# Kernel optimization log

Hardware: AMD Instinct MI355X
Metric: run time of the kernel (lower is better)

## Reference

```python
import jax, jax.numpy as jnp
import numpy as np

N = 50000      # nodes
E = 800000     # edges per relation (avg degree 16)
D = 128        # in_feat == out_feat
H = 4          # num_heads
DH = D // H    # head dim = 32
NEG_SLOPE = 0.2  # DGL GATConv default


def setup_inputs() -> dict:
    key = jax.random.key(0)
    ks = jax.random.split(key, 12)
    inp = {
        "x": jax.random.normal(ks[0], (N, D), jnp.float32),
        "W_r0": jax.random.normal(ks[1], (D, D), jnp.float32) * (1.0 / np.sqrt(D)),
        "attn_l_r0": jax.random.normal(ks[2], (H, DH), jnp.float32),
        "attn_r_r0": jax.random.normal(ks[3], (H, DH), jnp.float32),
        "W_r1": jax.random.normal(ks[4], (D, D), jnp.float32) * (1.0 / np.sqrt(D)),
        "attn_l_r1": jax.random.normal(ks[5], (H, DH), jnp.float32),
        "attn_r_r1": jax.random.normal(ks[6], (H, DH), jnp.float32),
        "loop_weight": jax.random.normal(ks[7], (D, D), jnp.float32) * (1.0 / np.sqrt(D)),
        "h_bias": jnp.zeros((D,), jnp.float32),
        "src_r0": jax.random.randint(ks[8], (E,), 0, N, jnp.int32),
        "dst_r0": jax.random.randint(ks[9], (E,), 0, N, jnp.int32),
        "src_r1": jax.random.randint(ks[10], (E,), 0, N, jnp.int32),
        "dst_r1": jax.random.randint(ks[11], (E,), 0, N, jnp.int32),
    }
    return inp


def _gat_conv(x, W, attn_l, attn_r, src, dst):
    """One DGL-style GATConv (no bias, no conv activation). Returns [N,H,DH]."""
    feat = (x @ W).reshape(N, H, DH)                 # projected features
    el = jnp.einsum('nhd,hd->nh', feat, attn_l)      # [N,H] attn on source
    er = jnp.einsum('nhd,hd->nh', feat, attn_r)      # [N,H] attn on dest
    e = jax.nn.leaky_relu(el[src] + er[dst], NEG_SLOPE)  # [E,H]
    # edge softmax over incoming edges of each dst node (stable)
    emax = jax.ops.segment_max(e, dst, num_segments=N)   # [N,H]
    ex = jnp.exp(e - emax[dst])                          # [E,H]
    denom = jax.ops.segment_sum(ex, dst, num_segments=N) # [N,H]
    alpha = ex / denom[dst]                              # [E,H]
    msg = feat[src] * alpha[:, :, None]                  # [E,H,DH]
    return jax.ops.segment_sum(msg, dst, num_segments=N) # [N,H,DH]


def reference(x, W_r0, attn_l_r0, attn_r_r0, W_r1, attn_l_r1, attn_r_r1,
              loop_weight, h_bias, src_r0, dst_r0, src_r1, dst_r1):
    # HeteroGraphConv with default 'sum' cross-relation aggregation
    h = _gat_conv(x, W_r0, attn_l_r0, attn_r_r0, src_r0, dst_r0) \
      + _gat_conv(x, W_r1, attn_l_r1, attn_r_r1, src_r1, dst_r1)
    h = h.reshape(N, H * DH)          # flatten heads -> [N, out_feat]
    h = h + x @ loop_weight           # self loop
    h = h + h_bias                    # bias
    h = jax.nn.relu(h)                # activation (dropout=0, no norm, no FFN)
    return h
```

## Files before the change

kernel.cpp:

```cpp
#include <hip/hip_runtime.h>
#include <hip/hip_bf16.h>

#define NN 50000
#define EE 800000
#define DD 128
#define HH 4
#define NEG_SLOPE 0.2f

#define BSH 9
#define NBUCK 98
#define CH 8192
#define NBLK 98
#define NSEG (2 * NBUCK * NBLK)
#define BKB (2 * NBLK)
#define PJB ((NN + 127) / 128)

typedef __attribute__((ext_vector_type(8))) short bf16x8;
typedef __attribute__((ext_vector_type(4))) float f32x4;
typedef __attribute__((ext_vector_type(8))) unsigned short ushrt8;

static __device__ __forceinline__ float bf2f(ushort u) {
    union { unsigned int ui; float f; } v; v.ui = ((unsigned int)u) << 16; return v.f;
}
static __device__ __forceinline__ void split1(float v, ushort& h, ushort& l) {
    __hip_bfloat16 hb = __float2bfloat16(v);
    float hf = __bfloat162float(hb);
    __hip_bfloat16 lb = __float2bfloat16(v - hf);
    h = *(ushort*)&hb; l = *(ushort*)&lb;
}

#define XB 6250
#define WB 192
__global__ __launch_bounds__(256) void prep_kernel(
    const float* __restrict__ x,
    const float* __restrict__ W0, const float* __restrict__ W1,
    const float* __restrict__ Wl,
    const int* __restrict__ dst0, const int* __restrict__ dst1,
    ushort* __restrict__ xh, ushort* __restrict__ xl, ushort* __restrict__ wt,
    int* __restrict__ hist)
{
    const int b = blockIdx.x;
    const int t = threadIdx.x;
    if (b < XB) {
        int i = b * 256 + t;
        float4 v = ((const float4*)x)[i];
        ushort4 h, l;
        split1(v.x, h.x, l.x); split1(v.y, h.y, l.y);
        split1(v.z, h.z, l.z); split1(v.w, h.w, l.w);
        *(ushort4*)&xh[(size_t)i * 4] = h;
        *(ushort4*)&xl[(size_t)i * 4] = l;
    } else if (b < XB + WB) {
        int idx = (b - XB) * 256 + t;
        int m = idx >> 14, e = idx & 16383;
        const float* W = (m == 0) ? W0 : (m == 1) ? W1 : Wl;
        int k = e >> 7, n = e & 127;
        ushort h, l; split1(W[e], h, l);
        int q = m * 4 + (k >> 5);
        int kin8 = (k >> 3) & 3, ke = k & 7;
        int sw = n & 7;
        size_t base = (size_t)q * 8192 + n * 64;
        wt[base + (((0 | kin8) ^ sw) << 3) + ke] = h;
        wt[base + (((4 | kin8) ^ sw) << 3) + ke] = l;
    } else {
        __shared__ int cnt[NBUCK];
        int hb = b - XB - WB;
        int rel = hb >= NBLK;
        int ci = hb - rel * NBLK;
        const int* __restrict__ dstA = rel ? dst1 : dst0;
        if (t < NBUCK) cnt[t] = 0;
        __syncthreads();
        int lo = ci * CH, hi = min(lo + CH, EE);
        for (int i = lo + t; i < hi; i += 256)
            atomicAdd(&cnt[dstA[i] >> BSH], 1);
        __syncthreads();
        if (t < NBUCK)
            hist[((rel * NBUCK) + t) * NBLK + ci] = cnt[t];
    }
}

__global__ __launch_bounds__(256) void scan_kernel(
    const int* __restrict__ hist, int* __restrict__ base)
{
    __shared__ int wq[4];
    const int t = threadIdx.x;
    const int lane = t & 63, wv = t >> 6;
    const int st = t * 76;
    const int en = min(st + 76, NSEG);
    int sum = 0;
    for (int i = st; i < en; ++i) sum += hist[i];
    int incl = sum;
    #pragma unroll
    for (int off = 1; off < 64; off <<= 1) {
        int u = __shfl_up(incl, off);
        if (lane >= off) incl += u;
    }
    if (lane == 63) wq[wv] = incl;
    __syncthreads();
    int woff = 0;
    #pragma unroll
    for (int w = 0; w < 4; ++w) woff += (w < wv) ? wq[w] : 0;
    int run = woff + incl - sum;
    for (int i = st; i < en; ++i) { base[i] = run; run += hist[i]; }
}

__global__ __launch_bounds__(256) void projbucket_kernel(
    const int* __restrict__ src0, const int* __restrict__ dst0,
    const int* __restrict__ src1, const int* __restrict__ dst1,
    const int* __restrict__ base, unsigned int* __restrict__ pk,
    const ushort* __restrict__ xh, const ushort* __restrict__ xl,
    const ushort* __restrict__ wt,
    const float* __restrict__ al0, const float* __restrict__ ar0,
    const float* __restrict__ al1, const float* __restrict__ ar1,
    const float* __restrict__ bias,
    ushort* __restrict__ fb0, ushort* __restrict__ fb1,
    float* __restrict__ el0, float* __restrict__ er0,
    float* __restrict__ el1, float* __restrict__ er1,
    float* __restrict__ out)
{
    __shared__ ushort lds[2][8192];
    const int t = threadIdx.x;

    if (blockIdx.x < BKB) {
        int* cnt = (int*)&lds[0][0];
        int* bs  = cnt + 128;
        const int hb = blockIdx.x;
        const int rel = hb >= NBLK;
        const int ci = hb - rel * NBLK;
        const int* __restrict__ srcA = rel ? src1 : src0;
        const int* __restrict__ dstA = rel ? dst1 : dst0;
        if (t < NBUCK) {
            cnt[t] = 0;
            bs[t] = base[((rel * NBUCK) + t) * NBLK + ci];
        }
        __syncthreads();
        int lo = ci * CH, hi = min(lo + CH, EE);
        for (int i = lo + t; i < hi; i += 256) {
            int dd = dstA[i], ss = srcA[i];
            int bk = dd >> BSH;
            int rk = atomicAdd(&cnt[bk], 1);
            pk[bs[bk] + rk] = (unsigned int)ss | ((unsigned int)(dd & 511) << 17);
        }
        return;
    }

    const int pb = blockIdx.x - BKB;
    const int lane = t & 63, wave = t >> 6;
    const int l15 = lane & 15, lg = lane >> 4;
    const int rb = pb * 128 + wave * 32;

    int ra0 = rb + l15;      if (ra0 > NN - 1) ra0 = NN - 1;
    int ra1 = rb + 16 + l15; if (ra1 > NN - 1) ra1 = NN - 1;
    const int kb = lg * 8;

    bf16x8 Ah0[4], Av0[4], Ah1[4], Av1[4];
    #pragma unroll
    for (int kc = 0; kc < 4; ++kc) {
        Ah0[kc] = *(const bf16x8*)&xh[(size_t)ra0 * DD + kc * 32 + kb];
        Av0[kc] = *(const bf16x8*)&xl[(size_t)ra0 * DD + kc * 32 + kb];
        Ah1[kc] = *(const bf16x8*)&xh[(size_t)ra1 * DD + kc * 32 + kb];
        Av1[kc] = *(const bf16x8*)&xl[(size_t)ra1 * DD + kc * 32 + kb];
    }

    {
        const bf16x8* g = (const bf16x8*)wt;
        bf16x8* L = (bf16x8*)lds[0];
        #pragma unroll
        for (int i = 0; i < 4; ++i) L[t + i * 256] = g[t + i * 256];
    }

    for (int m = 0; m < 3; ++m) {
        f32x4 acc0[8], acc1[8];
        #pragma unroll
        for (int nt = 0; nt < 8; ++nt) {
            acc0[nt] = (f32x4){0.f, 0.f, 0.f, 0.f};
            acc1[nt] = (f32x4){0.f, 0.f, 0.f, 0.f};
        }

        #pragma unroll
        for (int kc = 0; kc < 4; ++kc) {
            const int q = m * 4 + kc;
            __syncthreads();
            bf16x8 st0, st1, st2, st3;
            const bool hasNext = (q < 11);
            if (hasNext) {
                const bf16x8* g = (const bf16x8*)(wt + (size_t)(q + 1) * 8192);
                st0 = g[t]; st1 = g[t + 256]; st2 = g[t + 512]; st3 = g[t + 768];
            }
            const ushort* __restrict__ L = lds[kc & 1];
            #pragma unroll
            for (int nt = 0; nt < 8; ++nt) {
                const int n = nt * 16 + l15;
                const int sw = n & 7;
                bf16x8 bh = *(const bf16x8*)&L[n * 64 + (((0 | lg) ^ sw) << 3)];
                bf16x8 bv = *(const bf16x8*)&L[n * 64 + (((4 | lg) ^ sw) << 3)];
                acc0[nt] = __builtin_amdgcn_mfma_f32_16x16x32_bf16(Ah0[kc], bh, acc0[nt], 0, 0, 0);
                acc0[nt] = __builtin_amdgcn_mfma_f32_16x16x32_bf16(Ah0[kc], bv, acc0[nt], 0, 0, 0);
                acc0[nt] = __builtin_amdgcn_mfma_f32_16x16x32_bf16(Av0[kc], bh, acc0[nt], 0, 0, 0);
                acc1[nt] = __builtin_amdgcn_mfma_f32_16x16x32_bf16(Ah1[kc], bh, acc1[nt], 0, 0, 0);
                acc1[nt] = __builtin_amdgcn_mfma_f32_16x16x32_bf16(Ah1[kc], bv, acc1[nt], 0, 0, 0);
                acc1[nt] = __builtin_amdgcn_mfma_f32_16x16x32_bf16(Av1[kc], bh, acc1[nt], 0, 0, 0);
            }
            if (hasNext) {
                bf16x8* Lw = (bf16x8*)lds[(kc & 1) ^ 1];
                Lw[t] = st0; Lw[t + 256] = st1; Lw[t + 512] = st2; Lw[t + 768] = st3;
            }
        }

        if (m < 2) {
            ushort* __restrict__ fb = m ? fb1 : fb0;
            const float* __restrict__ alm = m ? al1 : al0;
            const float* __restrict__ arm = m ? ar1 : ar0;
            float* __restrict__ elm = m ? el1 : el0;
            float* __restrict__ erm = m ? er1 : er0;
            #pragma unroll
            for (int tt = 0; tt < 2; ++tt) {
                float pl[4][4], pr[4][4];
                #pragma unroll
                for (int r = 0; r < 4; ++r)
                    #pragma unroll
                    for (int h = 0; h < 4; ++h) { pl[r][h] = 0.f; pr[r][h] = 0.f; }
                #pragma unroll
                for (int nt = 0; nt < 8; ++nt) {
                    const int col = nt * 16 + l15;
                    const float wlv = alm[col], wrv = arm[col];
                    #pragma unroll
                    for (int r = 0; r < 4; ++r) {
                        const float v = tt ? acc1[nt][r] : acc0[nt][r];
                        pl[r][nt >> 1] += v * wlv;
                        pr[r][nt >> 1] += v * wrv;
                        const int row = rb + tt * 16 + lg * 4 + r;
                        if (row < NN) {
                            __hip_bfloat16 hb = __float2bfloat16(v);
                            fb[(size_t)row * DD + col] = *(ushort*)&hb;
                        }
                    }
                }
                #pragma unroll
                for (int msk = 1; msk < 16; msk <<= 1)
                    #pragma unroll
                    for (int r = 0; r < 4; ++r)
                        #pragma unroll
                        for (int h = 0; h < 4; ++h) {
                            pl[r][h] += __shfl_xor(pl[r][h], msk);
                            pr[r][h] += __shfl_xor(pr[r][h], msk);
                        }
                if (l15 < 4) {
                    #pragma unroll
                    for (int r = 0; r < 4; ++r) {
                        const int row = rb + tt * 16 + lg * 4 + r;
                        if (row < NN) {
                            const float plv = l15 == 0 ? pl[r][0] : l15 == 1 ? pl[r][1]
                                            : l15 == 2 ? pl[r][2] : pl[r][3];
                            const float prv = l15 == 0 ? pr[r][0] : l15 == 1 ? pr[r][1]
                                            : l15 == 2 ? pr[r][2] : pr[r][3];
                            elm[(size_t)row * 4 + l15] = plv;
                            erm[(size_t)row * 4 + l15] = prv;
                        }
                    }
                }
            }
        } else {
            #pragma unroll
            for (int tt = 0; tt < 2; ++tt)
                #pragma unroll
                for (int nt = 0; nt < 8; ++nt) {
                    const int col = nt * 16 + l15;
                    const float bv = bias[col];
                    #pragma unroll
                    for (int r = 0; r < 4; ++r) {
                        const int row = rb + tt * 16 + lg * 4 + r;
                        const float v = tt ? acc1[nt][r] : acc0[nt][r];
                        if (row < NN) out[(size_t)row * DD + col] = v + bv;
                    }
                }
        }
    }
}

__global__ __launch_bounds__(256) void sort_kernel(
    const unsigned int* __restrict__ pk, const int* __restrict__ base,
    int* __restrict__ row0, int* __restrict__ row1, int* __restrict__ list)
{
    __shared__ int cnt[512];
    __shared__ int offs[512];
    __shared__ int wq[4];
    const int hb = blockIdx.x;
    const int t = threadIdx.x;
    const int lane = t & 63, wv = t >> 6;
    const int rel = hb >= NBUCK;
    const int bk = hb - rel * NBUCK;

    const int fs = base[((rel * NBUCK) + bk) * NBLK];
    const int fe = (rel == 1 && bk == NBUCK - 1) ? 2 * EE
                 : base[((rel * NBUCK) + bk + 1) * NBLK];

    cnt[t] = 0; cnt[t + 256] = 0;
    __syncthreads();
    for (int i = fs + t; i < fe; i += 256)
        atomicAdd(&cnt[pk[i] >> 17], 1);
    __syncthreads();

    int a = cnt[2 * t], bvl = cnt[2 * t + 1];
    int ps = a + bvl;
    int incl = ps;
    #pragma unroll
    for (int off = 1; off < 64; off <<= 1) {
        int u = __shfl_up(incl, off);
        if (lane >= off) incl += u;
    }
    if (lane == 63) wq[wv] = incl;
    __syncthreads();
    int woff = 0;
    #pragma unroll
    for (int w = 0; w < 4; ++w) woff += (w < wv) ? wq[w] : 0;
    int excl = woff + incl - ps;
    offs[2 * t] = excl;
    offs[2 * t + 1] = excl + a;
    __syncthreads();

    int* __restrict__ row = rel ? row1 : row0;
    const int fsLocal = fs - (rel ? EE : 0);
    const int d0 = bk << BSH;
    for (int j = t; j < 512; j += 256) {
        int d = d0 + j;
        if (d < NN) row[d] = fsLocal + offs[j] + cnt[j];
    }
    __syncthreads();

    for (int i = fs + t; i < fe; i += 256) {
        unsigned int u = pk[i];
        int ld = u >> 17;
        int p = atomicAdd(&offs[ld], 1);
        list[fs + p] = (int)(u & 0x1FFFF);
    }
}

__global__ __launch_bounds__(256) void agg_kernel(
    const int* __restrict__ row0, const int* __restrict__ list0,
    const float* __restrict__ el0, const float* __restrict__ er0,
    const int* __restrict__ row1, const int* __restrict__ list1,
    const float* __restrict__ el1, const float* __restrict__ er1,
    const ushort* __restrict__ fb0, const ushort* __restrict__ fb1,
    float* __restrict__ out)
{
    const int d = blockIdx.x * 4 + (threadIdx.x >> 6);
    const int lane = threadIdx.x & 63;
    if (d >= NN) return;
    const int g = lane >> 4;
    const int l16 = lane & 15;
    const int c = l16 * 8;
    const int h = l16 >> 2;

    float tot[8] = {0.f, 0.f, 0.f, 0.f, 0.f, 0.f, 0.f, 0.f};

    #pragma unroll
    for (int rel = 0; rel < 2; ++rel) {
        const int* __restrict__ rowA = rel ? row1 : row0;
        const int* __restrict__ lst  = rel ? list1 : list0;
        const float* __restrict__ elA = rel ? el1 : el0;
        const float* __restrict__ erA = rel ? er1 : er0;
        const ushort* __restrict__ fbA = rel ? fb1 : fb0;

        const int s0 = d ? rowA[d - 1] : 0, e0 = rowA[d];
        const float erh = erA[(size_t)d * 4 + h];
        float acc[8] = {0.f, 0.f, 0.f, 0.f, 0.f, 0.f, 0.f, 0.f};
        float den = 0.f;

        int i = s0 + g;
        float elvA = 0.f;
        ushrt8 fA = (ushrt8){0, 0, 0, 0, 0, 0, 0, 0};
        if (i < e0) {
            int s = lst[i];
            elvA = elA[(size_t)s * 4 + h];
            fA = *(const ushrt8*)&fbA[(size_t)s * DD + c];
        }
        while (i < e0) {
            const int inext = i + 4;
            float elvB = 0.f;
            ushrt8 fB = (ushrt8){0, 0, 0, 0, 0, 0, 0, 0};
            if (inext < e0) {
                int s = lst[inext];
                elvB = elA[(size_t)s * 4 + h];
                fB = *(const ushrt8*)&fbA[(size_t)s * DD + c];
            }
            float ev = elvA + erh;
            ev = ev > 0.f ? ev : NEG_SLOPE * ev;
            float w = __expf(ev);
            den += w;
            #pragma unroll
            for (int q = 0; q < 8; ++q) acc[q] += w * bf2f(fA[q]);
            i = inext; elvA = elvB; fA = fB;
        }

        den += __shfl_xor(den, 16); den += __shfl_xor(den, 32);
        #pragma unroll
        for (int q = 0; q < 8; ++q) {
            acc[q] += __shfl_xor(acc[q], 16);
            acc[q] += __shfl_xor(acc[q], 32);
        }
        if (e0 > s0) {
            float inv = 1.f / den;
            #pragma unroll
            for (int q = 0; q < 8; ++q) tot[q] += acc[q] * inv;
        }
    }

    if (g == 0) {
        float4 o1 = *(float4*)&out[(size_t)d * DD + c];
        float4 o2 = *(float4*)&out[(size_t)d * DD + c + 4];
        o1.x = fmaxf(o1.x + tot[0], 0.f); o1.y = fmaxf(o1.y + tot[1], 0.f);
        o1.z = fmaxf(o1.z + tot[2], 0.f); o1.w = fmaxf(o1.w + tot[3], 0.f);
        o2.x = fmaxf(o2.x + tot[4], 0.f); o2.y = fmaxf(o2.y + tot[5], 0.f);
        o2.z = fmaxf(o2.z + tot[6], 0.f); o2.w = fmaxf(o2.w + tot[7], 0.f);
        *(float4*)&out[(size_t)d * DD + c] = o1;
        *(float4*)&out[(size_t)d * DD + c + 4] = o2;
    }
}

extern "C" void kernel_launch(void* const* d_in, const int* in_sizes, int n_in,
                              void* d_out, int out_size, void* d_ws, size_t ws_size,
                              hipStream_t stream)
{
    const float* x    = (const float*)d_in[0];
    const float* W0   = (const float*)d_in[1];
    const float* al0  = (const float*)d_in[2];
    const float* ar0  = (const float*)d_in[3];
    const float* W1   = (const float*)d_in[4];
    const float* al1  = (const float*)d_in[5];
    const float* ar1  = (const float*)d_in[6];
    const float* Wl   = (const float*)d_in[7];
    const float* bias = (const float*)d_in[8];
    const int* src0   = (const int*)d_in[9];
    const int* dst0   = (const int*)d_in[10];
    const int* src1   = (const int*)d_in[11];
    const int* dst1   = (const int*)d_in[12];
    float* out = (float*)d_out;

    ushort* wsu = (ushort*)d_ws;
    ushort* xh  = wsu;
    ushort* xl  = xh + (size_t)NN * DD;
    ushort* fb0 = xl + (size_t)NN * DD;
    ushort* fb1 = fb0 + (size_t)NN * DD;
    ushort* wt  = fb1 + (size_t)NN * DD;
    float* fbase = (float*)(wt + 12 * 8192);
    float* el0  = fbase;
    float* er0  = el0 + (size_t)NN * HH;
    float* el1  = er0 + (size_t)NN * HH;
    float* er1  = el1 + (size_t)NN * HH;
    int* hist   = (int*)(er1 + (size_t)NN * HH);
    int* base   = hist + NSEG;
    int* row0   = base + NSEG;
    int* row1   = row0 + NN;
    unsigned int* pk = (unsigned int*)(row1 + NN);
    int* list   = (int*)(pk + (size_t)2 * EE);
    int* list0  = list;
    int* list1  = list + EE;

    prep_kernel<<<dim3(XB + WB + 2 * NBLK), dim3(256), 0, stream>>>(
        x, W0, W1, Wl, dst0, dst1, xh, xl, wt, hist);

    scan_kernel<<<dim3(1), dim3(256), 0, stream>>>(hist, base);

    projbucket_kernel<<<dim3(BKB + PJB), dim3(256), 0, stream>>>(
        src0, dst0, src1, dst1, base, pk,
        xh, xl, wt, al0, ar0, al1, ar1, bias,
        fb0, fb1, el0, er0, el1, er1, out);

    sort_kernel<<<dim3(2 * NBUCK), dim3(256), 0, stream>>>(
        pk, base, row0, row1, list);

    agg_kernel<<<dim3((NN + 3) / 4), dim3(256), 0, stream>>>(
        row0, list0, el0, er0, row1, list1, el1, er1, fb0, fb1, out);
}
```

Baseline: 217.2 us.

## Precompute attention logits via W·a vectors and fuse softmax into sort

Folds attn_l/attn_r into the projection weights, so el/er come from x times precomputed 128-vectors in a separate light kernel rather than the MFMA epilogue. The edge softmax (exp, per-destination denominator, alpha) moves into the sort blocks, which now run concurrently with the projection GEMM in one launch. The aggregation reads precomputed alpha per edge instead of recomputing exp and denominators, and the x bf16 split moves inline into the GEMM so the separate x conversion pass and its buffers go away. This costs extra global traffic for the edge weight and alpha buffers (16 bytes per edge each), plus shared-memory float atomics, and el/er are computed with a different summation order.

After: 236.4 us. 8.9% more time.

```diff
diff --git a/kernel.cpp b/kernel.cpp
--- a/kernel.cpp
+++ b/kernel.cpp
@@ -13,7 +13,10 @@
 #define NBLK 98
 #define NSEG (2 * NBUCK * NBLK)
 #define BKB (2 * NBLK)
+#define SORTB (2 * NBUCK)
+#define ELRB 3125
 #define PJB ((NN + 127) / 128)
+#define WB 192
 
 typedef __attribute__((ext_vector_type(8))) short bf16x8;
 typedef __attribute__((ext_vector_type(4))) float f32x4;
@@ -29,28 +32,18 @@
     h = *(ushort*)&hb; l = *(ushort*)&lb;
 }
 
-#define XB 6250
-#define WB 192
 __global__ __launch_bounds__(256) void prep_kernel(
-    const float* __restrict__ x,
     const float* __restrict__ W0, const float* __restrict__ W1,
     const float* __restrict__ Wl,
+    const float* __restrict__ al0, const float* __restrict__ ar0,
+    const float* __restrict__ al1, const float* __restrict__ ar1,
     const int* __restrict__ dst0, const int* __restrict__ dst1,
-    ushort* __restrict__ xh, ushort* __restrict__ xl, ushort* __restrict__ wt,
-    int* __restrict__ hist)
+    ushort* __restrict__ wt, float* __restrict__ uvec, int* __restrict__ hist)
 {
     const int b = blockIdx.x;
     const int t = threadIdx.x;
-    if (b < XB) {
-        int i = b * 256 + t;
-        float4 v = ((const float4*)x)[i];
-        ushort4 h, l;
-        split1(v.x, h.x, l.x); split1(v.y, h.y, l.y);
-        split1(v.z, h.z, l.z); split1(v.w, h.w, l.w);
-        *(ushort4*)&xh[(size_t)i * 4] = h;
-        *(ushort4*)&xl[(size_t)i * 4] = l;
-    } else if (b < XB + WB) {
-        int idx = (b - XB) * 256 + t;
+    if (b < WB) {
+        int idx = b * 256 + t;
         int m = idx >> 14, e = idx & 16383;
         const float* W = (m == 0) ? W0 : (m == 1) ? W1 : Wl;
         int k = e >> 7, n = e & 127;
@@ -61,9 +54,9 @@
         size_t base = (size_t)q * 8192 + n * 64;
         wt[base + (((0 | kin8) ^ sw) << 3) + ke] = h;
         wt[base + (((4 | kin8) ^ sw) << 3) + ke] = l;
-    } else {
+    } else if (b < WB + BKB) {
         __shared__ int cnt[NBUCK];
-        int hb = b - XB - WB;
+        int hb = b - WB;
         int rel = hb >= NBLK;
         int ci = hb - rel * NBLK;
         const int* __restrict__ dstA = rel ? dst1 : dst0;
@@ -75,6 +68,19 @@
         __syncthreads();
         if (t < NBUCK)
             hist[((rel * NBUCK) + t) * NBLK + ci] = cnt[t];
+    } else {
+        #pragma unroll
+        for (int j = 0; j < 8; ++j) {
+            int idx = t * 8 + j;
+            int v = idx >> 7, k = idx & 127;
+            int rel = v >> 3, lr = (v >> 2) & 1, h = v & 3;
+            const float* W = rel ? W1 : W0;
+            const float* a = rel ? (lr ? ar1 : al1) : (lr ? ar0 : al0);
+            float s = 0.f;
+            for (int d2 = 0; d2 < 32; ++d2)
+                s += W[k * 128 + h * 32 + d2] * a[h * 32 + d2];
+            uvec[v * 128 + k] = s;
+        }
     }
 }
 
@@ -103,25 +109,19 @@
     for (int i = st; i < en; ++i) { base[i] = run; run += hist[i]; }
 }
 
-__global__ __launch_bounds__(256) void projbucket_kernel(
+__global__ __launch_bounds__(256) void bucketelr_kernel(
     const int* __restrict__ src0, const int* __restrict__ dst0,
     const int* __restrict__ src1, const int* __restrict__ dst1,
     const int* __restrict__ base, unsigned int* __restrict__ pk,
-    const ushort* __restrict__ xh, const ushort* __restrict__ xl,
-    const ushort* __restrict__ wt,
-    const float* __restrict__ al0, const float* __restrict__ ar0,
-    const float* __restrict__ al1, const float* __restrict__ ar1,
-    const float* __restrict__ bias,
-    ushort* __restrict__ fb0, ushort* __restrict__ fb1,
+    const float* __restrict__ x, const float* __restrict__ uvec,
     float* __restrict__ el0, float* __restrict__ er0,
-    float* __restrict__ el1, float* __restrict__ er1,
-    float* __restrict__ out)
+    float* __restrict__ el1, float* __restrict__ er1)
 {
-    __shared__ ushort lds[2][8192];
+    __shared__ float sm[2048];
     const int t = threadIdx.x;
 
     if (blockIdx.x < BKB) {
-        int* cnt = (int*)&lds[0][0];
+        int* cnt = (int*)sm;
         int* bs  = cnt + 128;
         const int hb = blockIdx.x;
         const int rel = hb >= NBLK;
@@ -143,7 +143,148 @@
         return;
     }
 
-    const int pb = blockIdx.x - BKB;
+    for (int i = t; i < 2048; i += 256) sm[i] = uvec[i];
+    __syncthreads();
+    const int lane = t & 63, wave = t >> 6;
+    const int l16 = lane & 15;
+    const int r = (blockIdx.x - BKB) * 16 + wave * 4 + (lane >> 4);
+    float xr[8];
+    if (r < NN) {
+        float4 a = *(const float4*)&x[(size_t)r * DD + l16 * 8];
+        float4 b2 = *(const float4*)&x[(size_t)r * DD + l16 * 8 + 4];
+        xr[0] = a.x; xr[1] = a.y; xr[2] = a.z; xr[3] = a.w;
+        xr[4] = b2.x; xr[5] = b2.y; xr[6] = b2.z; xr[7] = b2.w;
+    } else {
+        #pragma unroll
+        for (int j = 0; j < 8; ++j) xr[j] = 0.f;
+    }
+    float s[16];
+    #pragma unroll
+    for (int v = 0; v < 16; ++v) {
+        float acc = 0.f;
+        const float* u = &sm[v * 128 + l16 * 8];
+        #pragma unroll
+        for (int j = 0; j < 8; ++j) acc += xr[j] * u[j];
+        s[v] = acc;
+    }
+    #pragma unroll
+    for (int m = 1; m < 16; m <<= 1)
+        #pragma unroll
+        for (int v = 0; v < 16; ++v) s[v] += __shfl_xor(s[v], m);
+    if (r < NN) {
+        float val = s[0];
+        #pragma unroll
+        for (int v = 1; v < 16; ++v) val = (l16 == v) ? s[v] : val;
+        float* p = (l16 & 8) ? ((l16 & 4) ? er1 : el1)
+                             : ((l16 & 4) ? er0 : el0);
+        p[(size_t)r * 4 + (l16 & 3)] = val;
+    }
+}
+
+__global__ __launch_bounds__(256) void projsort_kernel(
+    const unsigned int* __restrict__ pk, const int* __restrict__ base,
+    const float* __restrict__ el0, const float* __restrict__ er0,
+    const float* __restrict__ el1, const float* __restrict__ er1,
+    float* __restrict__ wbuf,
+    int* __restrict__ row0, int* __restrict__ row1,
+    int* __restrict__ list, float* __restrict__ alphaAll,
+    const float* __restrict__ x, const ushort* __restrict__ wt,
+    const float* __restrict__ bias,
+    ushort* __restrict__ fb0, ushort* __restrict__ fb1,
+    float* __restrict__ out)
+{
+    __shared__ ushort lds[2][8192];
+    const int t = threadIdx.x;
+
+    if (blockIdx.x < SORTB) {
+        float* er_s = (float*)&lds[0][0];
+        float* den  = er_s + 2048;
+        int* cnt    = (int*)(den + 2048);
+        int* offs   = cnt + 512;
+        int* wq     = offs + 512;
+        const int hb = blockIdx.x;
+        const int lane = t & 63, wv = t >> 6;
+        const int rel = hb >= NBUCK;
+        const int bk = hb - rel * NBUCK;
+        const int fs = base[((rel * NBUCK) + bk) * NBLK];
+        const int fe = (rel == 1 && bk == NBUCK - 1) ? 2 * EE
+                     : base[((rel * NBUCK) + bk + 1) * NBLK];
+        const float* __restrict__ elA = rel ? el1 : el0;
+        const float* __restrict__ erA = rel ? er1 : er0;
+        const int d0 = bk << BSH;
+
+        for (int j = t; j < 512; j += 256) {
+            int d = d0 + j;
+            float4 e = make_float4(0.f, 0.f, 0.f, 0.f);
+            if (d < NN) e = *(const float4*)&erA[(size_t)d * 4];
+            *(float4*)&er_s[j * 4] = e;
+            *(float4*)&den[j * 4] = make_float4(0.f, 0.f, 0.f, 0.f);
+            cnt[j] = 0;
+        }
+        __syncthreads();
+
+        for (int i = fs + t; i < fe; i += 256) {
+            unsigned int u = pk[i];
+            int s = u & 0x1FFFF, ld = u >> 17;
+            atomicAdd(&cnt[ld], 1);
+            float4 e = *(const float4*)&elA[(size_t)s * 4];
+            float4 rr = *(const float4*)&er_s[ld * 4];
+            float4 w;
+            float v;
+            v = e.x + rr.x; v = v > 0.f ? v : NEG_SLOPE * v; w.x = __expf(v);
+            v = e.y + rr.y; v = v > 0.f ? v : NEG_SLOPE * v; w.y = __expf(v);
+            v = e.z + rr.z; v = v > 0.f ? v : NEG_SLOPE * v; w.z = __expf(v);
+            v = e.w + rr.w; v = v > 0.f ? v : NEG_SLOPE * v; w.w = __expf(v);
+            *(float4*)&wbuf[(size_t)i * 4] = w;
+            atomicAdd(&den[ld * 4 + 0], w.x);
+            atomicAdd(&den[ld * 4 + 1], w.y);
+            atomicAdd(&den[ld * 4 + 2], w.z);
+            atomicAdd(&den[ld * 4 + 3], w.w);
+        }
+        __syncthreads();
+
+        int a = cnt[2 * t], bvl = cnt[2 * t + 1];
+        int ps = a + bvl;
+        int incl = ps;
+        #pragma unroll
+        for (int off = 1; off < 64; off <<= 1) {
+            int u = __shfl_up(incl, off);
+            if (lane >= off) incl += u;
+        }
+        if (lane == 63) wq[wv] = incl;
+        __syncthreads();
+        int woff = 0;
+        #pragma unroll
+        for (int w = 0; w < 4; ++w) woff += (w < wv) ? wq[w] : 0;
+        int excl = woff + incl - ps;
+        offs[2 * t] = excl;
+        offs[2 * t + 1] = excl + a;
+        __syncthreads();
+
+        int* __restrict__ row = rel ? row1 : row0;
+        const int fsLocal = fs - (rel ? EE : 0);
+        for (int j = t; j < 512; j += 256) {
+            int d = d0 + j;
+            if (d < NN) row[d] = fsLocal + offs[j] + cnt[j];
+        }
+        for (int j = t; j < 2048; j += 256)
+            den[j] = 1.f / den[j];
+        __syncthreads();
+
+        for (int i = fs + t; i < fe; i += 256) {
+            unsigned int u = pk[i];
+            int s = u & 0x1FFFF, ld = u >> 17;
+            int p = atomicAdd(&offs[ld], 1);
+            float4 w = *(const float4*)&wbuf[(size_t)i * 4];
+            float4 dn = *(const float4*)&den[ld * 4];
+            float4 al4 = make_float4(w.x * dn.x, w.y * dn.y, w.z * dn.z, w.w * dn.w);
+            list[fs + p] = s;
+            *(float4*)&alphaAll[(size_t)(fs + p) * 4] = al4;
+        }
+        return;
+    }
+
+    const int pb = blockIdx.x - SORTB;
     const int lane = t & 63, wave = t >> 6;
     const int l15 = lane & 15, lg = lane >> 4;
     const int rb = pb * 128 + wave * 32;
@@ -155,10 +296,20 @@
     bf16x8 Ah0[4], Av0[4], Ah1[4], Av1[4];
     #pragma unroll
     for (int kc = 0; kc < 4; ++kc) {
-        Ah0[kc] = *(const bf16x8*)&xh[(size_t)ra0 * DD + kc * 32 + kb];
-        Av0[kc] = *(const bf16x8*)&xl[(size_t)ra0 * DD + kc * 32 + kb];
-        Ah1[kc] = *(const bf16x8*)&xh[(size_t)ra1 * DD + kc * 32 + kb];
-        Av1[kc] = *(const bf16x8*)&xl[(size_t)ra1 * DD + kc * 32 + kb];
+        const float* p0 = &x[(size_t)ra0 * DD + kc * 32 + kb];
+        const float* p1 = &x[(size_t)ra1 * DD + kc * 32 + kb];
+        float4 f0a = *(const float4*)p0, f0b = *(const float4*)(p0 + 4);
+        float4 f1a = *(const float4*)p1, f1b = *(const float4*)(p1 + 4);
+        float t0[8] = {f0a.x, f0a.y, f0a.z, f0a.w, f0b.x, f0b.y, f0b.z, f0b.w};
+        float t1[8] = {f1a.x, f1a.y, f1a.z, f1a.w, f1b.x, f1b.y, f1b.z, f1b.w};
+        union { bf16x8 v; ushort u[8]; } H0, L0, H1, L1;
+        #pragma unroll
+        for (int j = 0; j < 8; ++j) {
+            split1(t0[j], H0.u[j], L0.u[j]);
+            split1(t1[j], H1.u[j], L1.u[j]);
+        }
+        Ah0[kc] = H0.v; Av0[kc] = L0.v;
+        Ah1[kc] = H1.v; Av1[kc] = L1.v;
     }
 
     {
@@ -208,57 +359,21 @@
 
         if (m < 2) {
             ushort* __restrict__ fb = m ? fb1 : fb0;
-            const float* __restrict__ alm = m ? al1 : al0;
-            const float* __restrict__ arm = m ? ar1 : ar0;
-            float* __restrict__ elm = m ? el1 : el0;
-            float* __restrict__ erm = m ? er1 : er0;
             #pragma unroll
-            for (int tt = 0; tt < 2; ++tt) {
-                float pl[4][4], pr[4][4];
-                #pragma unroll
-                for (int r = 0; r < 4; ++r)
-                    #pragma unroll
-                    for (int h = 0; h < 4; ++h) { pl[r][h] = 0.f; pr[r][h] = 0.f; }
+            for (int tt = 0; tt < 2; ++tt)
                 #pragma unroll
                 for (int nt = 0; nt < 8; ++nt) {
                     const int col = nt * 16 + l15;
-                    const float wlv = alm[col], wrv = arm[col];
                     #pragma unroll
                     for (int r = 0; r < 4; ++r) {
+                        const int row = rb + tt * 16 + lg * 4 + r;
                         const float v = tt ? acc1[nt][r] : acc0[nt][r];
-                        pl[r][nt >> 1] += v * wlv;
-                        pr[r][nt >> 1] += v * wrv;
-                        const int row = rb + tt * 16 + lg * 4 + r;
                         if (row < NN) {
                             __hip_bfloat16 hb = __float2bfloat16(v);
                             fb[(size_t)row * DD + col] = *(ushort*)&hb;
                         }
                     }
                 }
-                #pragma unroll
-                for (int msk = 1; msk < 16; msk <<= 1)
-                    #pragma unroll
-                    for (int r = 0; r < 4; ++r)
-                        #pragma unroll
-                        for (int h = 0; h < 4; ++h) {
-                            pl[r][h] += __shfl_xor(pl[r][h], msk);
-                            pr[r][h] += __shfl_xor(pr[r][h], msk);
-                        }
-                if (l15 < 4) {
-                    #pragma unroll
-                    for (int r = 0; r < 4; ++r) {
-                        const int row = rb + tt * 16 + lg * 4 + r;
-                        if (row < NN) {
-                            const float plv = l15 == 0 ? pl[r][0] : l15 == 1 ? pl[r][1]
-                                            : l15 == 2 ? pl[r][2] : pl[r][3];
-                            const float prv = l15 == 0 ? pr[r][0] : l15 == 1 ? pr[r][1]
-                                            : l15 == 2 ? pr[r][2] : pr[r][3];
-                            elm[(size_t)row * 4 + l15] = plv;
-                            erm[(size_t)row * 4 + l15] = prv;
-                        }
-                    }
-                }
-            }
         } else {
             #pragma unroll
             for (int tt = 0; tt < 2; ++tt)
@@ -277,69 +392,10 @@
     }
 }
 
-__global__ __launch_bounds__(256) void sort_kernel(
-    const unsigned int* __restrict__ pk, const int* __restrict__ base,
-    int* __restrict__ row0, int* __restrict__ row1, int* __restrict__ list)
-{
-    __shared__ int cnt[512];
-    __shared__ int offs[512];
-    __shared__ int wq[4];
-    const int hb = blockIdx.x;
-    const int t = threadIdx.x;
-    const int lane = t & 63, wv = t >> 6;
-    const int rel = hb >= NBUCK;
-    const int bk = hb - rel * NBUCK;
-
-    const int fs = base[((rel * NBUCK) + bk) * NBLK];
-    const int fe = (rel == 1 && bk == NBUCK - 1) ? 2 * EE
-                 : base[((rel * NBUCK) + bk + 1) * NBLK];
-
-    cnt[t] = 0; cnt[t + 256] = 0;
-    __syncthreads();
-    for (int i = fs + t; i < fe; i += 256)
-        atomicAdd(&cnt[pk[i] >> 17], 1);
-    __syncthreads();
-
-    int a = cnt[2 * t], bvl = cnt[2 * t + 1];
-    int ps = a + bvl;
-    int incl = ps;
-    #pragma unroll
-    for (int off = 1; off < 64; off <<= 1) {
-        int u = __shfl_up(incl, off);
-        if (lane >= off) incl += u;
-    }
-    if (lane == 63) wq[wv] = incl;
-    __syncthreads();
-    int woff = 0;
-    #pragma unroll
-    for (int w = 0; w < 4; ++w) woff += (w < wv) ? wq[w] : 0;
-    int excl = woff + incl - ps;
-    offs[2 * t] = excl;
-    offs[2 * t + 1] = excl + a;
-    __syncthreads();
-
-    int* __restrict__ row = rel ? row1 : row0;
-    const int fsLocal = fs - (rel ? EE : 0);
-    const int d0 = bk << BSH;
-    for (int j = t; j < 512; j += 256) {
-        int d = d0 + j;
-        if (d < NN) row[d] = fsLocal + offs[j] + cnt[j];
-    }
-    __syncthreads();
-
-    for (int i = fs + t; i < fe; i += 256) {
-        unsigned int u = pk[i];
-        int ld = u >> 17;
-        int p = atomicAdd(&offs[ld], 1);
-        list[fs + p] = (int)(u & 0x1FFFF);
-    }
-}
-
 __global__ __launch_bounds__(256) void agg_kernel(
     const int* __restrict__ row0, const int* __restrict__ list0,
-    const float* __restrict__ el0, const float* __restrict__ er0,
     const int* __restrict__ row1, const int* __restrict__ list1,
-    const float* __restrict__ el1, const float* __restrict__ er1,
+    const float* __restrict__ alphaAll,
     const ushort* __restrict__ fb0, const ushort* __restrict__ fb1,
     float* __restrict__ out)
 {
@@ -357,51 +413,39 @@
     for (int rel = 0; rel < 2; ++rel) {
         const int* __restrict__ rowA = rel ? row1 : row0;
         const int* __restrict__ lst  = rel ? list1 : list0;
-        const float* __restrict__ elA = rel ? el1 : el0;
-        const float* __restrict__ erA = rel ? er1 : er0;
         const ushort* __restrict__ fbA = rel ? fb1 : fb0;
+        const size_t ab = rel ? (size_t)EE : 0;
 
         const int s0 = d ? rowA[d - 1] : 0, e0 = rowA[d];
-        const float erh = erA[(size_t)d * 4 + h];
         float acc[8] = {0.f, 0.f, 0.f, 0.f, 0.f, 0.f, 0.f, 0.f};
-        float den = 0.f;
 
         int i = s0 + g;
-        float elvA = 0.f;
+        float aA = 0.f;
         ushrt8 fA = (ushrt8){0, 0, 0, 0, 0, 0, 0, 0};
         if (i < e0) {
             int s = lst[i];
-            elvA = elA[(size_t)s * 4 + h];
+            aA = alphaAll[(ab + (size_t)i) * 4 + h];
             fA = *(const ushrt8*)&fbA[(size_t)s * DD + c];
         }
         while (i < e0) {
             const int inext = i + 4;
-            float elvB = 0.f;
+            float aB = 0.f;
             ushrt8 fB = (ushrt8){0, 0, 0, 0, 0, 0, 0, 0};
             if (inext < e0) {
                 int s = lst[inext];
-                elvB = elA[(size_t)s * 4 + h];
+                aB = alphaAll[(ab + (size_t)inext) * 4 + h];
                 fB = *(const ushrt8*)&fbA[(size_t)s * DD + c];
             }
-            float ev = elvA + erh;
-            ev = ev > 0.f ? ev : NEG_SLOPE * ev;
-            float w = __expf(ev);
-            den += w;
             #pragma unroll
-            for (int q = 0; q < 8; ++q) acc[q] += w * bf2f(fA[q]);
-            i = inext; elvA = elvB; fA = fB;
-        }
-
-        den += __shfl_xor(den, 16); den += __shfl_xor(den, 32);
+            for (int q = 0; q < 8; ++q) acc[q] += aA * bf2f(fA[q]);
+            i = inext; aA = aB; fA = fB;
+        }
+
         #pragma unroll
         for (int q = 0; q < 8; ++q) {
             acc[q] += __shfl_xor(acc[q], 16);
             acc[q] += __shfl_xor(acc[q], 32);
-        }
-        if (e0 > s0) {
-            float inv = 1.f / den;
-            #pragma unroll
-            for (int q = 0; q < 8; ++q) tot[q] += acc[q] * inv;
+            tot[q] += acc[q];
         }
     }
 
@@ -436,14 +480,14 @@
     const int* dst1   = (const int*)d_in[12];
     float* out = (float*)d_out;
 
-    ushort* wsu = (ushort*)d_ws;
-    ushort* xh  = wsu;
-    ushort* xl  = xh + (size_t)NN * DD;
-    ushort* fb0 = xl + (size_t)NN * DD;
+    float* wsf      = (float*)d_ws;
+    float* wbuf     = wsf;
+    float* alphaAll = wbuf + (size_t)8 * EE;
+    ushort* fb0 = (ushort*)(alphaAll + (size_t)8 * EE);
     ushort* fb1 = fb0 + (size_t)NN * DD;
     ushort* wt  = fb1 + (size_t)NN * DD;
-    float* fbase = (float*)(wt + 12 * 8192);
-    float* el0  = fbase;
+    float* uvec = (float*)(wt + 12 * 8192);
+    float* el0  = uvec + 2048;
     float* er0  = el0 + (size_t)NN * HH;
     float* el1  = er0 + (size_t)NN * HH;
     float* er1  = el1 + (size_t)NN * HH;
@@ -456,19 +500,18 @@
     int* list0  = list;
     int* list1  = list + EE;
 
-    prep_kernel<<<dim3(XB + WB + 2 * NBLK), dim3(256), 0, stream>>>(
-        x, W0, W1, Wl, dst0, dst1, xh, xl, wt, hist);
+    prep_kernel<<<dim3(WB + BKB + 1), dim3(256), 0, stream>>>(
+        W0, W1, Wl, al0, ar0, al1, ar1, dst0, dst1, wt, uvec, hist);
 
     scan_kernel<<<dim3(1), dim3(256), 0, stream>>>(hist, base);
 
-    projbucket_kernel<<<dim3(BKB + PJB), dim3(256), 0, stream>>>(
-        src0, dst0, src1, dst1, base, pk,
-        xh, xl, wt, al0, ar0, al1, ar1, bias,
-        fb0, fb1, el0, er0, el1, er1, out);
-
-    sort_kernel<<<dim3(2 * NBUCK), dim3(256), 0, stream>>>(
-        pk, base, row0, row1, list);
+    bucketelr_kernel<<<dim3(BKB + ELRB), dim3(256), 0, stream>>>(
+        src0, dst0, src1, dst1, base, pk, x, uvec, el0, er0, el1, er1);
+
+    projsort_kernel<<<dim3(SORTB + PJB), dim3(256), 0, stream>>>(
+        pk, base, el0, er0, el1, er1, wbuf, row0, row1, list, alphaAll,
+        x, wt, bias, fb0, fb1, out);
 
     agg_kernel<<<dim3((NN + 3) / 4), dim3(256), 0, stream>>>(
-        row0, list0, el0, er0, row1, list1, el1, er1, fb0, fb1, out);
-}
+        row0, list0, row1, list1, alphaAll, fb0, fb1, out);
+}
```
